# Optimization experiments

Measured on AMD Instinct MI355X. Metric: run time of the kernel, lower is better.

## Reference

```python
import jax, jax.numpy as jnp
import numpy as np

B = 131072   # batch rows in the (pooled) sparse tensor
C = 512      # conv_out4
J = 7        # jnt_dim
H = 512      # linear_out
TAU_MAX = 1.0  # undefined global in source; torque cap, taken as 1.0
EPS = 1e-5


def layer_norm(x, g, b):
    m = jnp.mean(x, axis=-1, keepdims=True)
    v = jnp.var(x, axis=-1, keepdims=True)
    return (x - m) * jax.lax.rsqrt(v + EPS) * g + b


def setup_inputs() -> dict:
    key = jax.random.key(0)
    ks = jax.random.split(key, 6)
    return {
        "features": jax.random.normal(ks[0], (B, C), dtype=jnp.float32),
        "coords": jax.random.randint(ks[1], (B,), 0, B),  # batch indices (col 0 of ME coords)
        "jnt_pos": jax.random.normal(ks[2], (B, J), dtype=jnp.float32),
        "jnt_goal": jax.random.normal(ks[3], (B, J), dtype=jnp.float32),
        "ln1_g": jnp.ones((C,), jnp.float32),
        "ln1_b": jnp.zeros((C,), jnp.float32),
        "W1": jax.random.normal(ks[4], (C + 2 * J, H), dtype=jnp.float32) / np.sqrt(C + 2 * J),
        "b1": jnp.zeros((H,), jnp.float32),
        "ln2_g": jnp.ones((H,), jnp.float32),
        "ln2_b": jnp.zeros((H,), jnp.float32),
        "W2": jax.random.normal(ks[5], (H, J), dtype=jnp.float32) / np.sqrt(H),
        "b2": jnp.zeros((J,), jnp.float32),
    }


def reference(features, coords, jnt_pos, jnt_goal,
              ln1_g, ln1_b, W1, b1, ln2_g, ln2_b, W2, b2):
    # to_dense_tnsr: y = zeros_like(features); for c in coords: y[c] = features[c]
    # vectorized: single gather + scatter (duplicate writes carry identical values)
    y = jnp.zeros_like(features).at[coords].set(features[coords])
    # norm = LayerNorm(512) -> SELU   (dropout in eval mode: identity)
    x = jax.nn.selu(layer_norm(y, ln1_g, ln1_b))
    # cat((jnt_pos, jnt_goal, x), dim=1)
    x = jnp.concatenate([jnt_pos, jnt_goal, x], axis=1)  # [B, 2J+C]
    # linear = Linear -> LayerNorm -> SELU
    x = jax.nn.selu(layer_norm(x @ W1 + b1, ln2_g, ln2_b))
    # out = Linear -> Tanh, scaled by tau_max
    return jnp.tanh(x @ W2 + b2) * TAU_MAX
```

## Files before the change

kernel.cpp:

```cpp
#include <hip/hip_runtime.h>

#define B_ROWS   131072
#define MTILE    64
#define KCHUNKS  17
#define LDA      552
#define LDX      528
#define W1F_OFF  ((size_t)B_ROWS)
#define W2F_OFF  (W1F_OFF + (size_t)544 * 512 * 2)

typedef _Float16 f16x8 __attribute__((ext_vector_type(8)));
typedef float    f32x4 __attribute__((ext_vector_type(4)));

__device__ inline unsigned short f2h(float f) {
  _Float16 h = (_Float16)f;
  return __builtin_bit_cast(unsigned short, h);
}
__device__ inline float h2f(unsigned short u) {
  return (float)__builtin_bit_cast(_Float16, u);
}
__device__ inline float selu_f(float x) {
  const float lam = 1.0507009873554805f, alp = 1.6732632423543772f;
  return x > 0.f ? lam * x : lam * alp * (__expf(x) - 1.f);
}

__global__ void scatter_mask(const int* __restrict__ coords,
                             unsigned char* __restrict__ mask) {
  int i = blockIdx.x * 256 + threadIdx.x;
  mask[coords[i]] = 1u;
}

__global__ void build_wf(const float* __restrict__ W1, const float* __restrict__ W2,
                         unsigned short* __restrict__ W1f, unsigned short* __restrict__ W2f) {
  int tid = threadIdx.x;
  if (blockIdx.x < 544) {
    int fragIdx = blockIdx.x;
    int ni = fragIdx & 3;
    int c  = (fragIdx >> 2) % 17;
    int wq = fragIdx / 68;
    int nbase = wq * 64 + ni * 16;
    __shared__ float t[32][17];
    int kl = tid >> 4, nl = tid & 15;
    int kg = c * 32 + kl;
    float v = 0.f;
    if (kg < 512)      v = W1[(size_t)(kg + 14) * 512 + nbase + nl];
    else if (kg < 526) v = W1[(size_t)(kg - 512) * 512 + nbase + nl];
    t[kl][nl] = v;
    __syncthreads();
    int lane = tid >> 3, e = tid & 7;
    int k2 = ((lane >> 4) & 3) * 8 + e;
    int n2 = lane & 15;
    W1f[(size_t)fragIdx * 512 + tid] = f2h(t[k2][n2]);
  } else {
    int c2 = blockIdx.x - 544;
    int lane = tid >> 3, e = tid & 7;
    int n = lane & 15, quad = (lane >> 4) & 3;
    int k = c2 * 32 + quad * 8 + e;
    float v = (n < 7) ? W2[(size_t)k * 7 + n] : 0.f;
    W2f[(size_t)c2 * 512 + tid] = f2h(v);
  }
}

struct __align__(16) SMem {
  char buf[70656];
  float part[8][MTILE][2];
  float mean2[MTILE], rstd2[MTILE];
};

__global__ __launch_bounds__(512, 4) void actor_main(
    const float* __restrict__ feat, const unsigned char* __restrict__ mask,
    const float* __restrict__ jp, const float* __restrict__ jg,
    const float* __restrict__ ln1g, const float* __restrict__ ln1b,
    const unsigned short* __restrict__ W1f, const float* __restrict__ b1,
    const float* __restrict__ ln2g, const float* __restrict__ ln2b,
    const unsigned short* __restrict__ W2f, const float* __restrict__ b2,
    float* __restrict__ out) {
  __shared__ SMem sm;
  unsigned short* At = (unsigned short*)sm.buf;
  unsigned short* X2 = (unsigned short*)sm.buf;
  float*          O  = (float*)(sm.buf + 64 * LDX * 2);

  const int tid  = threadIdx.x;
  const int wq   = tid >> 6;
  const int lane = tid & 63;
  const int m0   = blockIdx.x * MTILE;
  const int mrow = lane & 15;
  const int quad = lane >> 4;

  const int arow = tid >> 3;
  const int acg  = tid & 7;
  {
    const int row  = m0 + arow;
    float mk = mask[row] ? 1.f : 0.f;
    const float4* frow = (const float4*)feat + (size_t)row * 128 + acg;
    float s = 0.f, q = 0.f;
#pragma unroll
    for (int c = 0; c < 16; ++c) {
      float4 v = frow[(size_t)c * 8];
      s += v.x + v.y + v.z + v.w;
      q += v.x * v.x + v.y * v.y + v.z * v.z + v.w * v.w;
      union { unsigned short us[4]; uint2 u; } pk;
      pk.us[0] = f2h(v.x * mk); pk.us[1] = f2h(v.y * mk);
      pk.us[2] = f2h(v.z * mk); pk.us[3] = f2h(v.w * mk);
      *(uint2*)&At[arow * LDA + c * 32 + acg * 4] = pk.u;
    }
    {
      union { unsigned short us[4]; uint2 u; } pk;
#pragma unroll
      for (int q2 = 0; q2 < 4; ++q2) {
        int kk = acg * 4 + q2;
        float val = 0.f;
        if (kk < 7)       val = jp[(size_t)row * 7 + kk];
        else if (kk < 14) val = jg[(size_t)row * 7 + kk - 7];
        pk.us[q2] = f2h(val);
      }
      *(uint2*)&At[arow * LDA + 512 + acg * 4] = pk.u;
    }
    s += __shfl_xor(s, 1); q += __shfl_xor(q, 1);
    s += __shfl_xor(s, 2); q += __shfl_xor(q, 2);
    s += __shfl_xor(s, 4); q += __shfl_xor(q, 4);
    float mean = mk * s * (1.f / 512.f);
    float msq  = mk * q * (1.f / 512.f);
    float rstd = rsqrtf(msq - mean * mean + 1e-5f);

#pragma unroll
    for (int c = 0; c < 16; ++c) {
      union { unsigned short us[4]; uint2 u; } w;
      w.u = *(uint2*)&At[arow * LDA + c * 32 + acg * 4];
      float4 g = ((const float4*)ln1g)[c * 8 + acg];
      float4 b = ((const float4*)ln1b)[c * 8 + acg];
      union { unsigned short us[4]; uint2 u; } pk;
      pk.us[0] = f2h(selu_f((h2f(w.us[0]) - mean) * rstd * g.x + b.x));
      pk.us[1] = f2h(selu_f((h2f(w.us[1]) - mean) * rstd * g.y + b.y));
      pk.us[2] = f2h(selu_f((h2f(w.us[2]) - mean) * rstd * g.z + b.z));
      pk.us[3] = f2h(selu_f((h2f(w.us[3]) - mean) * rstd * g.w + b.w));
      *(uint2*)&At[arow * LDA + c * 32 + acg * 4] = pk.u;
    }
  }

  const unsigned short* wBase = W1f + (size_t)wq * 68 * 512 + lane * 8;
  f16x8 bE[4], bO[4];
#pragma unroll
  for (int ni = 0; ni < 4; ++ni)
    bE[ni] = *(const f16x8*)(wBase + (size_t)ni * 512);

  __syncthreads();

  f32x4 acc[4][4];
#pragma unroll
  for (int mi = 0; mi < 4; ++mi)
#pragma unroll
    for (int ni = 0; ni < 4; ++ni) acc[mi][ni] = (f32x4){0.f, 0.f, 0.f, 0.f};

  const unsigned short* aB = At + mrow * LDA + quad * 8;

  auto loadB = [&](f16x8* dst, int c) {
#pragma unroll
    for (int ni = 0; ni < 4; ++ni)
      dst[ni] = *(const f16x8*)(wBase + (size_t)(c * 4 + ni) * 512);
  };
  auto step = [&](const f16x8* bF, int c) {
    f16x8 a[4];
#pragma unroll
    for (int mi = 0; mi < 4; ++mi)
      a[mi] = *(const f16x8*)(aB + mi * 16 * LDA + c * 32);
#pragma unroll
    for (int mi = 0; mi < 4; ++mi)
#pragma unroll
      for (int ni = 0; ni < 4; ++ni)
        acc[mi][ni] = __builtin_amdgcn_mfma_f32_16x16x32_f16(a[mi], bF[ni], acc[mi][ni], 0, 0, 0);
  };

  for (int c = 0; c < KCHUNKS - 1; c += 2) {
    loadB(bO, c + 1);
    step(bE, c);
    loadB(bE, c + 2);
    step(bO, c + 1);
  }
  step(bE, 16);

  f16x8 bW2[2];
  bW2[0] = *(const f16x8*)&W2f[(size_t)(2 * wq)     * 512 + lane * 8];
  bW2[1] = *(const f16x8*)&W2f[(size_t)(2 * wq + 1) * 512 + lane * 8];

  float b1v[4], g2v[4], bl2v[4];
#pragma unroll
  for (int ni = 0; ni < 4; ++ni) {
    int col = wq * 64 + ni * 16 + mrow;
    b1v[ni] = b1[col]; g2v[ni] = ln2g[col]; bl2v[ni] = ln2b[col];
  }
#pragma unroll
  for (int mi = 0; mi < 4; ++mi)
#pragma unroll
    for (int reg = 0; reg < 4; ++reg) {
      int r = mi * 16 + quad * 4 + reg;
      float s = 0.f, q = 0.f;
#pragma unroll
      for (int ni = 0; ni < 4; ++ni) {
        float v = acc[mi][ni][reg] + b1v[ni];
        acc[mi][ni][reg] = v;
        s += v; q += v * v;
      }
      s += __shfl_xor(s, 1); q += __shfl_xor(q, 1);
      s += __shfl_xor(s, 2); q += __shfl_xor(q, 2);
      s += __shfl_xor(s, 4); q += __shfl_xor(q, 4);
      s += __shfl_xor(s, 8); q += __shfl_xor(q, 8);
      if ((lane & 15) == 0) { sm.part[wq][r][0] = s; sm.part[wq][r][1] = q; }
    }
  __syncthreads();
  if (tid < MTILE) {
    float s = 0.f, q = 0.f;
#pragma unroll
    for (int w = 0; w < 8; ++w) { s += sm.part[w][tid][0]; q += sm.part[w][tid][1]; }
    float mean = s * (1.f / 512.f);
    float var  = q * (1.f / 512.f) - mean * mean;
    sm.mean2[tid] = mean;
    sm.rstd2[tid] = rsqrtf(var + 1e-5f);
  }
  O[tid] = 0.f;
  __syncthreads();
#pragma unroll
  for (int mi = 0; mi < 4; ++mi)
#pragma unroll
    for (int ni = 0; ni < 4; ++ni)
#pragma unroll
      for (int reg = 0; reg < 4; ++reg) {
        int r = mi * 16 + quad * 4 + reg;
        int col = wq * 64 + ni * 16 + mrow;
        float v = (acc[mi][ni][reg] - sm.mean2[r]) * sm.rstd2[r] * g2v[ni] + bl2v[ni];
        X2[r * LDX + col] = f2h(selu_f(v));
      }
  __syncthreads();

  {
    f32x4 acc2[4];
#pragma unroll
    for (int mi = 0; mi < 4; ++mi) acc2[mi] = (f32x4){0.f, 0.f, 0.f, 0.f};
#pragma unroll
    for (int j = 0; j < 2; ++j) {
      int c2 = 2 * wq + j;
#pragma unroll
      for (int mi = 0; mi < 4; ++mi) {
        f16x8 a = *(const f16x8*)&X2[(mi * 16 + mrow) * LDX + c2 * 32 + quad * 8];
        acc2[mi] = __builtin_amdgcn_mfma_f32_16x16x32_f16(a, bW2[j], acc2[mi], 0, 0, 0);
      }
    }
#pragma unroll
    for (int mi = 0; mi < 4; ++mi)
#pragma unroll
      for (int reg = 0; reg < 4; ++reg)
        if (mrow < 7)
          atomicAdd(&O[(mi * 16 + quad * 4 + reg) * 8 + mrow], acc2[mi][reg]);
  }
  __syncthreads();
  {
    int r = tid >> 3, c = tid & 7;
    if (c < 7)
      out[(size_t)(m0 + r) * 7 + c] = tanhf(O[tid] + b2[c]);
  }
}

extern "C" void kernel_launch(void* const* d_in, const int* in_sizes, int n_in,
                              void* d_out, int out_size, void* d_ws, size_t ws_size,
                              hipStream_t stream) {
  const float* feat  = (const float*)d_in[0];
  const int*   crd   = (const int*)d_in[1];
  const float* jp    = (const float*)d_in[2];
  const float* jg    = (const float*)d_in[3];
  const float* ln1g  = (const float*)d_in[4];
  const float* ln1b  = (const float*)d_in[5];
  const float* W1    = (const float*)d_in[6];
  const float* b1    = (const float*)d_in[7];
  const float* ln2g  = (const float*)d_in[8];
  const float* ln2b  = (const float*)d_in[9];
  const float* W2    = (const float*)d_in[10];
  const float* b2    = (const float*)d_in[11];
  float* out = (float*)d_out;

  unsigned char*  mask = (unsigned char*)d_ws;
  unsigned short* W1f  = (unsigned short*)((char*)d_ws + W1F_OFF);
  unsigned short* W2f  = (unsigned short*)((char*)d_ws + W2F_OFF);

  hipMemsetAsync(mask, 0, (size_t)B_ROWS, stream);
  scatter_mask<<<B_ROWS / 256, 256, 0, stream>>>(crd, mask);
  build_wf<<<560, 512, 0, stream>>>(W1, W2, W1f, W2f);
  actor_main<<<B_ROWS / MTILE, 512, 0, stream>>>(
      feat, mask, jp, jg, ln1g, ln1b, W1f, b1, ln2g, ln2b, W2f, b2, out);
}
```

Measured before the change: 512.8 us.

## Split LayerNorm1 row statistics into a separate pre-pass kernel

Adds a row_stats kernel that streams the feature matrix once to compute per-row mean and rstd into workspace. The main GEMM kernel then reads those stats and applies LN1+SELU in a single pass over the features, so it no longer needs the two-pass fp16 staging through LDS. This shortens the prologue of the occupancy-limited GEMM kernel. In exchange the 256 MB feature matrix is read twice from HBM, and there is an extra kernel launch.

Result: slower. 562.9 us (+9.8%).

```diff
diff --git a/kernel.cpp b/kernel.cpp
--- a/kernel.cpp
+++ b/kernel.cpp
@@ -5,18 +5,18 @@
 #define KCHUNKS  17
 #define LDA      552
 #define LDX      528
-#define W1F_OFF  ((size_t)B_ROWS)
-#define W2F_OFF  (W1F_OFF + (size_t)544 * 512 * 2)
+#define STATS_GRID 2048
+#define W1F_OFF   ((size_t)B_ROWS)
+#define W2F_OFF   (W1F_OFF + (size_t)544 * 512 * 2)
+#define STATS_OFF (W2F_OFF + (size_t)16 * 512 * 2)
 
 typedef _Float16 f16x8 __attribute__((ext_vector_type(8)));
 typedef float    f32x4 __attribute__((ext_vector_type(4)));
+typedef float    fv4   __attribute__((ext_vector_type(4)));
 
 __device__ inline unsigned short f2h(float f) {
   _Float16 h = (_Float16)f;
   return __builtin_bit_cast(unsigned short, h);
-}
-__device__ inline float h2f(unsigned short u) {
-  return (float)__builtin_bit_cast(_Float16, u);
 }
 __device__ inline float selu_f(float x) {
   const float lam = 1.0507009873554805f, alp = 1.6732632423543772f;
@@ -60,21 +60,44 @@
   }
 }
 
-struct __align__(16) SMem {
+__global__ __launch_bounds__(512) void row_stats(
+    const float* __restrict__ feat, float2* __restrict__ stats) {
+  const int w = threadIdx.x >> 6, lane = threadIdx.x & 63;
+#pragma unroll 1
+  for (int it = 0; it < B_ROWS / (STATS_GRID * 8); ++it) {
+    const size_t row = (size_t)(it * STATS_GRID + blockIdx.x) * 8 + w;
+    const fv4* frow = (const fv4*)feat + row * 128;
+    fv4 f0 = __builtin_nontemporal_load(frow + lane);
+    fv4 f1 = __builtin_nontemporal_load(frow + 64 + lane);
+    float s = f0.x + f0.y + f0.z + f0.w + f1.x + f1.y + f1.z + f1.w;
+    float q = f0.x * f0.x + f0.y * f0.y + f0.z * f0.z + f0.w * f0.w +
+              f1.x * f1.x + f1.y * f1.y + f1.z * f1.z + f1.w * f1.w;
+#pragma unroll
+    for (int d = 32; d > 0; d >>= 1) { s += __shfl_xor(s, d); q += __shfl_xor(q, d); }
+    if (lane == 0) {
+      float mean = s * (1.f / 512.f);
+      float var  = q * (1.f / 512.f) - mean * mean;
+      stats[row] = make_float2(mean, rsqrtf(var + 1e-5f));
+    }
+  }
+}
+
+struct __align__(16) SMemG {
   char buf[70656];
   float part[8][MTILE][2];
   float mean2[MTILE], rstd2[MTILE];
 };
 
-__global__ __launch_bounds__(512, 4) void actor_main(
+__global__ __launch_bounds__(512, 4) void actor_gemm(
     const float* __restrict__ feat, const unsigned char* __restrict__ mask,
+    const float2* __restrict__ stats,
     const float* __restrict__ jp, const float* __restrict__ jg,
     const float* __restrict__ ln1g, const float* __restrict__ ln1b,
     const unsigned short* __restrict__ W1f, const float* __restrict__ b1,
     const float* __restrict__ ln2g, const float* __restrict__ ln2b,
     const unsigned short* __restrict__ W2f, const float* __restrict__ b2,
     float* __restrict__ out) {
-  __shared__ SMem sm;
+  __shared__ SMemG sm;
   unsigned short* At = (unsigned short*)sm.buf;
   unsigned short* X2 = (unsigned short*)sm.buf;
   float*          O  = (float*)(sm.buf + 64 * LDX * 2);
@@ -86,21 +109,24 @@
   const int mrow = lane & 15;
   const int quad = lane >> 4;
 
-  const int arow = tid >> 3;
-  const int acg  = tid & 7;
   {
+    const int arow = tid >> 3;
+    const int acg  = tid & 7;
     const int row  = m0 + arow;
+    float2 st = stats[row];
     float mk = mask[row] ? 1.f : 0.f;
+    float mm = st.x, rm = st.y * mk;
     const float4* frow = (const float4*)feat + (size_t)row * 128 + acg;
-    float s = 0.f, q = 0.f;
-#pragma unroll
+#pragma unroll 4
     for (int c = 0; c < 16; ++c) {
-      float4 v = frow[(size_t)c * 8];
-      s += v.x + v.y + v.z + v.w;
-      q += v.x * v.x + v.y * v.y + v.z * v.z + v.w * v.w;
+      float4 f = frow[(size_t)c * 8];
+      float4 g = ((const float4*)ln1g)[c * 8 + acg];
+      float4 b = ((const float4*)ln1b)[c * 8 + acg];
       union { unsigned short us[4]; uint2 u; } pk;
-      pk.us[0] = f2h(v.x * mk); pk.us[1] = f2h(v.y * mk);
-      pk.us[2] = f2h(v.z * mk); pk.us[3] = f2h(v.w * mk);
+      pk.us[0] = f2h(selu_f((f.x - mm) * rm * g.x + b.x));
+      pk.us[1] = f2h(selu_f((f.y - mm) * rm * g.y + b.y));
+      pk.us[2] = f2h(selu_f((f.z - mm) * rm * g.z + b.z));
+      pk.us[3] = f2h(selu_f((f.w - mm) * rm * g.w + b.w));
       *(uint2*)&At[arow * LDA + c * 32 + acg * 4] = pk.u;
     }
     {
@@ -114,26 +140,6 @@
         pk.us[q2] = f2h(val);
       }
       *(uint2*)&At[arow * LDA + 512 + acg * 4] = pk.u;
-    }
-    s += __shfl_xor(s, 1); q += __shfl_xor(q, 1);
-    s += __shfl_xor(s, 2); q += __shfl_xor(q, 2);
-    s += __shfl_xor(s, 4); q += __shfl_xor(q, 4);
-    float mean = mk * s * (1.f / 512.f);
-    float msq  = mk * q * (1.f / 512.f);
-    float rstd = rsqrtf(msq - mean * mean + 1e-5f);
-
-#pragma unroll
-    for (int c = 0; c < 16; ++c) {
-      union { unsigned short us[4]; uint2 u; } w;
-      w.u = *(uint2*)&At[arow * LDA + c * 32 + acg * 4];
-      float4 g = ((const float4*)ln1g)[c * 8 + acg];
-      float4 b = ((const float4*)ln1b)[c * 8 + acg];
-      union { unsigned short us[4]; uint2 u; } pk;
-      pk.us[0] = f2h(selu_f((h2f(w.us[0]) - mean) * rstd * g.x + b.x));
-      pk.us[1] = f2h(selu_f((h2f(w.us[1]) - mean) * rstd * g.y + b.y));
-      pk.us[2] = f2h(selu_f((h2f(w.us[2]) - mean) * rstd * g.z + b.z));
-      pk.us[3] = f2h(selu_f((h2f(w.us[3]) - mean) * rstd * g.w + b.w));
-      *(uint2*)&At[arow * LDA + c * 32 + acg * 4] = pk.u;
     }
   }
 
@@ -276,13 +282,15 @@
   const float* b2    = (const float*)d_in[11];
   float* out = (float*)d_out;
 
-  unsigned char*  mask = (unsigned char*)d_ws;
-  unsigned short* W1f  = (unsigned short*)((char*)d_ws + W1F_OFF);
-  unsigned short* W2f  = (unsigned short*)((char*)d_ws + W2F_OFF);
-
-  hipMemsetAsync(mask, 0, (size_t)B_ROWS, stream);
+  unsigned char*  mask  = (unsigned char*)d_ws;
+  unsigned short* W1f   = (unsigned short*)((char*)d_ws + W1F_OFF);
+  unsigned short* W2f   = (unsigned short*)((char*)d_ws + W2F_OFF);
+  float2*         stats = (float2*)((char*)d_ws + STATS_OFF);
+
+  (void)hipMemsetAsync(mask, 0, (size_t)B_ROWS, stream);
   scatter_mask<<<B_ROWS / 256, 256, 0, stream>>>(crd, mask);
   build_wf<<<560, 512, 0, stream>>>(W1, W2, W1f, W2f);
-  actor_main<<<B_ROWS / MTILE, 512, 0, stream>>>(
-      feat, mask, jp, jg, ln1g, ln1b, W1f, b1, ln2g, ln2b, W2f, b2, out);
-}
+  row_stats<<<STATS_GRID, 512, 0, stream>>>(feat, stats);
+  actor_gemm<<<B_ROWS / MTILE, 512, 0, stream>>>(
+      feat, mask, stats, jp, jg, ln1g, ln1b, W1f, b1, ln2g, ln2b, W2f, b2, out);
+}
```
